# Kernel tuning notes

Hardware: AMD Instinct MI355X
Metric: run time of the kernel (lower is better)

## Reference

```python
import jax, jax.numpy as jnp
import numpy as np

C = 32                      # channels
DIMS = (8, 14, 18)          # basis_dim_per_atom for the 3 atom types
COUNTS = (8192, 8192, 4096) # number of atoms of each type


def setup_inputs() -> dict:
    key = jax.random.key(0)
    ks = iter(jax.random.split(key, 32))
    inp = {}
    N = sum(d * n for d, n in zip(DIMS, COUNTS))  # 253952 total basis rows
    inp["x"] = jax.random.normal(next(ks), (N, C), jnp.float32)
    c2 = C * C
    off = 0
    for t, (d, n) in enumerate(zip(DIMS, COUNTS)):
        rows = d * n
        # index array equivalent to the boolean atomic_number_mask for this type
        inp[f"idx{t}"] = jnp.arange(off, off + rows, dtype=jnp.int32)
        off += rows
        A = jax.random.normal(next(ks), (d, d), jnp.float32)
        inp[f"S{t}"] = 0.1 * (A + A.T)  # symmetric Coulomb/overlap matrix stand-in
        inp[f"W1_{t}"] = jax.random.normal(next(ks), (c2, c2), jnp.float32) * 0.03
        inp[f"b1_{t}"] = jnp.zeros((c2,), jnp.float32)
        inp[f"g{t}"] = jnp.ones((c2,), jnp.float32)
        inp[f"beta{t}"] = jnp.zeros((c2,), jnp.float32)
        inp[f"W2_{t}"] = jax.random.normal(next(ks), (c2, c2), jnp.float32) * 0.03
        inp[f"b2_{t}"] = jnp.zeros((c2,), jnp.float32)
    return inp


def _atom_block(y, S, W1, b1, g, beta, W2, b2):
    # y: [n_atoms, d, C]
    n = y.shape[0]
    # l2 = einsum('ij,aic,ajm->acm', S, y, y)  -> [n, C, C]
    Sy = jnp.einsum('ij,ajm->aim', S, y)
    l2 = jnp.einsum('aic,aim->acm', y, Sy)
    h = l2.reshape(n, C * C)
    # MLP: Linear -> SiLU -> LayerNorm -> Linear
    h = jax.nn.silu(h @ W1.T + b1)
    mu = jnp.mean(h, axis=-1, keepdims=True)
    var = jnp.var(h, axis=-1, keepdims=True)
    h = (h - mu) * jax.lax.rsqrt(var + 1e-5) * g + beta
    l2 = (h @ W2.T + b2).reshape(n, C, C)
    # x = x @ l2 per atom
    return jnp.einsum('aic,acm->aim', y, l2)


def reference(x, idx0, idx1, idx2,
              S0, W1_0, b1_0, g0, beta0, W2_0, b2_0,
              S1, W1_1, b1_1, g1, beta1, W2_1, b2_1,
              S2, W1_2, b1_2, g2, beta2, W2_2, b2_2):
    idxs = (idx0, idx1, idx2)
    params = ((S0, W1_0, b1_0, g0, beta0, W2_0, b2_0),
              (S1, W1_1, b1_1, g1, beta1, W2_1, b2_1),
              (S2, W1_2, b1_2, g2, beta2, W2_2, b2_2))
    for t in range(3):  # fixed small loop over atom types (structurally distinct)
        d = DIMS[t]
        y = x[idxs[t]].reshape(-1, d, C)          # gather + view per atom
        out = _atom_block(y, *params[t])          # per-type sub-module
        x = x.at[idxs[t]].set(out.reshape(-1, C)) # scatter back
    return x
```

## Files before the change

kernel.cpp:

```cpp
#include <hip/hip_runtime.h>
#include <math.h>

#define C2 1024

typedef float f32x4 __attribute__((ext_vector_type(4)));
typedef _Float16 f16x8 __attribute__((ext_vector_type(8)));
typedef unsigned short u16x8 __attribute__((ext_vector_type(8)));

__device__ __forceinline__ unsigned short f2h(float f) {
    _Float16 h = (_Float16)f;
    return __builtin_bit_cast(unsigned short, h);
}

__device__ __forceinline__ void gload16(const void* g, void* l) {
    __builtin_amdgcn_global_load_lds((const __attribute__((address_space(1))) void*)g,
                                     (__attribute__((address_space(3))) void*)l,
                                     16, 0, 0);
}

__device__ __forceinline__ int type_of(int pos, int s1, int s2) {
    return (pos >= s2) ? 2 : (pos >= s1) ? 1 : 0;
}
__device__ __forceinline__ int dim_of(int t) { return (t == 0) ? 8 : (t == 1) ? 14 : 18; }

__global__ __launch_bounds__(256) void k_conv(const float* __restrict__ s0, const float* __restrict__ s1,
                                              const float* __restrict__ s2, const float* __restrict__ s3,
                                              const float* __restrict__ s4, const float* __restrict__ s5,
                                              unsigned short* __restrict__ w) {
    int mat = blockIdx.x >> 10, bb = blockIdx.x & 1023;
    const float* src = (mat == 0) ? s0 : (mat == 1) ? s1 : (mat == 2) ? s2
                       : (mat == 3) ? s3 : (mat == 4) ? s4 : s5;
    int i = (bb * 256 + threadIdx.x) * 4;
    unsigned short* dst = w + (size_t)mat * 1048576;
    float4 v = *(const float4*)(src + i);
    ushort4 h;
    h.x = f2h(v.x); h.y = f2h(v.y); h.z = f2h(v.z); h.w = f2h(v.w);
    *(ushort4*)(dst + i) = h;
}

__global__ __launch_bounds__(256) void k_l2(const float* __restrict__ x,
                                            const int* __restrict__ i0, const int* __restrict__ i1,
                                            const int* __restrict__ i2,
                                            const float* __restrict__ S0, const float* __restrict__ S1,
                                            const float* __restrict__ S2,
                                            unsigned short* __restrict__ Ah,
                                            int s1, int s2) {
    __shared__ float sS[324];
    __shared__ float sy[4][18][32];
    __shared__ float sSy[4][18][32];
    const int tid = threadIdx.x, g = tid >> 6, lane = tid & 63;
    const int a0 = blockIdx.x * 4;
    const int t = type_of(a0, s1, s2);
    const int d = dim_of(t);
    const int* idx = (t == 0) ? i0 : (t == 1) ? i1 : i2;
    const float* S = (t == 0) ? S0 : (t == 1) ? S1 : S2;
    const int start = (t == 0) ? 0 : (t == 1) ? s1 : s2;
    const int dd = d * d;
    for (int i = tid; i < dd; i += 256) sS[i] = S[i];
    const int a = a0 + g, la = a - start;
    const int nf4 = d * 8;
    for (int k = lane; k < nf4; k += 64) {
        int bi = k >> 3, f4 = (k & 7) * 4;
        int r = idx[la * d + bi];
        *(float4*)&sy[g][bi][f4] = *(const float4*)(x + (size_t)r * 32 + f4);
    }
    __syncthreads();
    for (int k = lane; k < d * 32; k += 64) {
        int i = k >> 5, m = k & 31;
        float acc = 0.f;
        for (int j = 0; j < d; ++j) acc += sS[i * d + j] * sy[g][j][m];
        sSy[g][i][m] = acc;
    }
    __syncthreads();
    const int c = lane >> 1, mb = (lane & 1) * 16;
    float acc[16];
#pragma unroll
    for (int mm = 0; mm < 16; ++mm) acc[mm] = 0.f;
    for (int i = 0; i < d; ++i) {
        float yc = sy[g][i][c];
#pragma unroll
        for (int mm = 0; mm < 16; ++mm) acc[mm] += yc * sSy[g][i][mb + mm];
    }
    u16x8 h0, h1;
#pragma unroll
    for (int mm = 0; mm < 8; ++mm) h0[mm] = f2h(acc[mm]);
#pragma unroll
    for (int mm = 0; mm < 8; ++mm) h1[mm] = f2h(acc[8 + mm]);
    size_t off = (size_t)a * C2 + lane * 16;
    *(u16x8*)(Ah + off) = h0;
    *(u16x8*)(Ah + off + 8) = h1;
}

template <int DO_SILU>
__global__ __launch_bounds__(256) void k_gemm_mfma(const unsigned short* __restrict__ A,
                                                   const unsigned short* __restrict__ W0,
                                                   const unsigned short* __restrict__ W1,
                                                   const unsigned short* __restrict__ W2,
                                                   const float* __restrict__ bias0, const float* __restrict__ bias1,
                                                   const float* __restrict__ bias2,
                                                   float* __restrict__ Out, int tb1, int tb2) {
    __shared__ short lds[8192];
    short* As = lds;
    short* Ws = lds + 4096;

    const int tid = threadIdx.x;
    const int wid = tid >> 6, lane = tid & 63;
    const int bm = blockIdx.x, bn = blockIdx.y;
    const int wr = wid >> 1, wc = wid & 1;

    const unsigned short* W; const float* bias;
    if (bm >= tb2)      { W = W2; bias = bias2; }
    else if (bm >= tb1) { W = W1; bias = bias1; }
    else                { W = W0; bias = bias0; }

    size_t gA[2], gW[2];
    int ldsoff[2];
#pragma unroll
    for (int it = 0; it < 2; ++it) {
        int L = wid * 128 + it * 64 + lane;
        int row = L >> 2, slot = L & 3;
        int sw = slot ^ ((row >> 1) & 3);
        gA[it] = (size_t)(bm * 128 + row) * C2 + sw * 8;
        gW[it] = (size_t)(bn * 128 + row) * C2 + sw * 8;
        ldsoff[it] = wid * 1024 + it * 512;
    }

    const int col = lane & 15, g = lane >> 4;
    int aoffs[4], woffs[4];
#pragma unroll
    for (int i = 0; i < 4; ++i) {
        int ra = wr * 64 + i * 16 + col;
        aoffs[i] = ra * 32 + (g ^ ((ra >> 1) & 3)) * 8;
        int rw = wc * 64 + i * 16 + col;
        woffs[i] = rw * 32 + (g ^ ((rw >> 1) & 3)) * 8;
    }

    f32x4 acc[4][4] = {};

    for (int k0 = 0; k0 < C2; k0 += 32) {
#pragma unroll
        for (int it = 0; it < 2; ++it) {
            gload16(A + gA[it] + k0, As + ldsoff[it]);
            gload16(W + gW[it] + k0, Ws + ldsoff[it]);
        }
        __syncthreads();
        f16x8 ah[4], wh[4];
#pragma unroll
        for (int i = 0; i < 4; ++i) {
            ah[i] = *(const f16x8*)(As + aoffs[i]);
            wh[i] = *(const f16x8*)(Ws + woffs[i]);
        }
#pragma unroll
        for (int mi = 0; mi < 4; ++mi)
#pragma unroll
            for (int ni = 0; ni < 4; ++ni)
                acc[mi][ni] = __builtin_amdgcn_mfma_f32_16x16x32_f16(ah[mi], wh[ni], acc[mi][ni], 0, 0, 0);
        __syncthreads();
    }

    float bv[4];
#pragma unroll
    for (int ni = 0; ni < 4; ++ni) bv[ni] = bias[bn * 128 + wc * 64 + ni * 16 + col];
#pragma unroll
    for (int mi = 0; mi < 4; ++mi)
#pragma unroll
        for (int ni = 0; ni < 4; ++ni) {
            int n = bn * 128 + wc * 64 + ni * 16 + col;
#pragma unroll
            for (int r = 0; r < 4; ++r) {
                int m = bm * 128 + wr * 64 + mi * 16 + g * 4 + r;
                float v = acc[mi][ni][r] + bv[ni];
                if (DO_SILU) v = v / (1.f + __expf(-v));
                Out[(size_t)m * C2 + n] = v;
            }
        }
}

__global__ __launch_bounds__(256) void k_ln(const float* __restrict__ H,
                                            const float* __restrict__ g0, const float* __restrict__ g1,
                                            const float* __restrict__ g2,
                                            const float* __restrict__ b0, const float* __restrict__ b1,
                                            const float* __restrict__ b2,
                                            unsigned short* __restrict__ Bh,
                                            int s1, int s2) {
    const int tid = threadIdx.x, w = tid >> 6, lane = tid & 63;
    const int row = blockIdx.x * 4 + w;
    const int t = type_of(row, s1, s2);
    const float* gg = (t == 0) ? g0 : (t == 1) ? g1 : g2;
    const float* bb = (t == 0) ? b0 : (t == 1) ? b1 : b2;
    const float* rp = H + (size_t)row * C2;
    float4 v[4];
    float s = 0.f, s2v = 0.f;
#pragma unroll
    for (int k = 0; k < 4; ++k) {
        v[k] = *(const float4*)(rp + k * 256 + lane * 4);
        s += v[k].x + v[k].y + v[k].z + v[k].w;
        s2v += v[k].x * v[k].x + v[k].y * v[k].y + v[k].z * v[k].z + v[k].w * v[k].w;
    }
#pragma unroll
    for (int off = 1; off < 64; off <<= 1) {
        s += __shfl_xor(s, off);
        s2v += __shfl_xor(s2v, off);
    }
    float mean = s * (1.f / 1024.f);
    float var = s2v * (1.f / 1024.f) - mean * mean;
    float rstd = rsqrtf(var + 1e-5f);
#pragma unroll
    for (int k = 0; k < 4; ++k) {
        float4 gv = *(const float4*)(gg + k * 256 + lane * 4);
        float4 bv = *(const float4*)(bb + k * 256 + lane * 4);
        ushort4 h;
        h.x = f2h((v[k].x - mean) * rstd * gv.x + bv.x);
        h.y = f2h((v[k].y - mean) * rstd * gv.y + bv.y);
        h.z = f2h((v[k].z - mean) * rstd * gv.z + bv.z);
        h.w = f2h((v[k].w - mean) * rstd * gv.w + bv.w);
        size_t off2 = (size_t)row * C2 + k * 256 + lane * 4;
        *(ushort4*)(Bh + off2) = h;
    }
}

__global__ __launch_bounds__(256) void k_out(const float* __restrict__ x,
                                             const int* __restrict__ i0, const int* __restrict__ i1,
                                             const int* __restrict__ i2,
                                             const float* __restrict__ L,
                                             float* __restrict__ out, int s1, int s2) {
    __shared__ float sL[4][C2];
    __shared__ float sy[4][18][32];
    const int tid = threadIdx.x, g = tid >> 6, lane = tid & 63;
    const int a0 = blockIdx.x * 4;
    const int t = type_of(a0, s1, s2);
    const int d = dim_of(t);
    const int* idx = (t == 0) ? i0 : (t == 1) ? i1 : i2;
    const int start = (t == 0) ? 0 : (t == 1) ? s1 : s2;
    const int a = a0 + g, la = a - start;
    for (int k = lane; k < 256; k += 64)
        *(float4*)&sL[g][k * 4] = *(const float4*)(L + (size_t)a * C2 + k * 4);
    const int nf4 = d * 8;
    for (int k = lane; k < nf4; k += 64) {
        int bi = k >> 3, f4 = (k & 7) * 4;
        int r = idx[la * d + bi];
        *(float4*)&sy[g][bi][f4] = *(const float4*)(x + (size_t)r * 32 + f4);
    }
    __syncthreads();
    for (int k = lane; k < nf4; k += 64) {
        int bi = k >> 3, m4 = (k & 7) * 4;
        float ax = 0.f, ay = 0.f, az = 0.f, aw = 0.f;
#pragma unroll
        for (int c = 0; c < 32; ++c) {
            float yv = sy[g][bi][c];
            float4 lv = *(const float4*)&sL[g][c * 32 + m4];
            ax += yv * lv.x; ay += yv * lv.y; az += yv * lv.z; aw += yv * lv.w;
        }
        int r = idx[la * d + bi];
        float4 o = {ax, ay, az, aw};
        *(float4*)(out + (size_t)r * 32 + m4) = o;
    }
}

extern "C" void kernel_launch(void* const* d_in, const int* in_sizes, int n_in,
                              void* d_out, int out_size, void* d_ws, size_t ws_size,
                              hipStream_t stream) {
    const float* x = (const float*)d_in[0];
    static const int DIMS[3] = {8, 14, 18};
    static const int NATOMS[3] = {8192, 8192, 4096};
    const size_t MiB = 1ull << 20;
    const int BIG = 0x40000000;
    char* p = (char*)d_ws;

    const int* idxs[3]; const float* Ss[3]; const float* W1s[3]; const float* b1s[3];
    const float* gs[3]; const float* bes[3]; const float* W2s[3]; const float* b2s[3];
    for (int t = 0; t < 3; ++t) {
        idxs[t] = (const int*)d_in[1 + 8 * t];
        Ss[t] = (const float*)d_in[2 + 8 * t];
        W1s[t] = (const float*)d_in[3 + 8 * t];
        b1s[t] = (const float*)d_in[4 + 8 * t];
        gs[t] = (const float*)d_in[5 + 8 * t];
        bes[t] = (const float*)d_in[6 + 8 * t];
        W2s[t] = (const float*)d_in[7 + 8 * t];
        b2s[t] = (const float*)d_in[8 + 8 * t];
    }
    float* outp = (float*)d_out;

    if (ws_size >= 132 * MiB) {
        unsigned short* w = (unsigned short*)p;
        unsigned short* Ah = (unsigned short*)(p + 12 * MiB);
        float* H = (float*)(p + 52 * MiB);
        k_conv<<<6 * 1024, 256, 0, stream>>>(W1s[0], W2s[0], W1s[1], W2s[1], W1s[2], W2s[2], w);
        k_l2<<<5120, 256, 0, stream>>>(x, idxs[0], idxs[1], idxs[2], Ss[0], Ss[1], Ss[2],
                                       Ah, 8192, 16384);
        dim3 gg(160, 8);
        k_gemm_mfma<1><<<gg, 256, 0, stream>>>(Ah,
            w + 0 * 1048576, w + 2 * 1048576, w + 4 * 1048576,
            b1s[0], b1s[1], b1s[2], H, 64, 128);
        k_ln<<<5120, 256, 0, stream>>>(H, gs[0], gs[1], gs[2], bes[0], bes[1], bes[2],
                                       Ah, 8192, 16384);
        k_gemm_mfma<0><<<gg, 256, 0, stream>>>(Ah,
            w + 1 * 1048576, w + 3 * 1048576, w + 5 * 1048576,
            b2s[0], b2s[1], b2s[2], H, 64, 128);
        k_out<<<5120, 256, 0, stream>>>(x, idxs[0], idxs[1], idxs[2], H, outp, 8192, 16384);
    } else {
        unsigned short* wt = (unsigned short*)p;
        char* dyn = p + 4 * MiB;
        for (int t = 0; t < 3; ++t) {
            int n = NATOMS[t], d = DIMS[t];
            size_t fullneed = 4 * MiB + (size_t)n * 6144;
            int nch = (ws_size >= fullneed) ? 1 : 2;
            int cm = n / nch;
            unsigned short* Ah = (unsigned short*)dyn;
            float* Hbuf = (float*)(dyn + (size_t)cm * 2048);
            int ss1 = (t == 0) ? BIG : 0;
            int ss2 = (t == 2) ? 0 : BIG;
            k_conv<<<2 * 1024, 256, 0, stream>>>(W1s[t], W2s[t], W1s[t], W1s[t], W1s[t], W1s[t], wt);
            for (int ch = 0; ch < nch; ++ch) {
                const int* idxc = idxs[t] + (size_t)(ch * cm) * d;
                k_l2<<<cm / 4, 256, 0, stream>>>(x, idxc, idxc, idxc, Ss[t], Ss[t], Ss[t],
                                                 Ah, ss1, ss2);
                dim3 g1(cm / 128, 8);
                k_gemm_mfma<1><<<g1, 256, 0, stream>>>(Ah,
                    wt + 0, wt + 0, wt + 0,
                    b1s[t], b1s[t], b1s[t], Hbuf, BIG, BIG);
                k_ln<<<cm / 4, 256, 0, stream>>>(Hbuf, gs[t], gs[t], gs[t], bes[t], bes[t], bes[t],
                                                 Ah, ss1, ss2);
                k_gemm_mfma<0><<<g1, 256, 0, stream>>>(Ah,
                    wt + 1048576, wt + 1048576, wt + 1048576,
                    b2s[t], b2s[t], b2s[t], Hbuf, BIG, BIG);
                k_out<<<cm / 4, 256, 0, stream>>>(x, idxc, idxc, idxc, Hbuf, outp, ss1, ss2);
            }
        }
    }
    (void)in_sizes; (void)n_in; (void)out_size;
}
```

Before: 330.1 us.

## Store GEMM outputs as fp16 via LDS-staged coalesced writes

The two MLP GEMMs now write their intermediate activations in fp16 instead of fp32, and the epilogue stages each tile through padded LDS so global stores are 16-byte coalesced. LayerNorm and the output kernel read fp16 and convert back to fp32. This halves the intermediate activation traffic and removes scattered 4-byte stores, at the cost of extra epilogue syncs and reduced precision in the pre-LayerNorm and final l2 values.

Result: no change. 329.9 us (-0.1%).

```diff
diff --git a/kernel.cpp b/kernel.cpp
--- a/kernel.cpp
+++ b/kernel.cpp
@@ -10,6 +10,9 @@
 __device__ __forceinline__ unsigned short f2h(float f) {
     _Float16 h = (_Float16)f;
     return __builtin_bit_cast(unsigned short, h);
+}
+__device__ __forceinline__ float h2f(unsigned short u) {
+    return (float)__builtin_bit_cast(_Float16, u);
 }
 
 __device__ __forceinline__ void gload16(const void* g, void* l) {
@@ -98,8 +101,8 @@
                                                    const unsigned short* __restrict__ W2,
                                                    const float* __restrict__ bias0, const float* __restrict__ bias1,
                                                    const float* __restrict__ bias2,
-                                                   float* __restrict__ Out, int tb1, int tb2) {
-    __shared__ short lds[8192];
+                                                   unsigned short* __restrict__ Out, int tb1, int tb2) {
+    __shared__ short lds[8704];
     short* As = lds;
     short* Ws = lds + 4096;
 
@@ -161,22 +164,39 @@
     float bv[4];
 #pragma unroll
     for (int ni = 0; ni < 4; ++ni) bv[ni] = bias[bn * 128 + wc * 64 + ni * 16 + col];
-#pragma unroll
-    for (int mi = 0; mi < 4; ++mi)
-#pragma unroll
-        for (int ni = 0; ni < 4; ++ni) {
-            int n = bn * 128 + wc * 64 + ni * 16 + col;
-#pragma unroll
-            for (int r = 0; r < 4; ++r) {
-                int m = bm * 128 + wr * 64 + mi * 16 + g * 4 + r;
-                float v = acc[mi][ni][r] + bv[ni];
-                if (DO_SILU) v = v / (1.f + __expf(-v));
-                Out[(size_t)m * C2 + n] = v;
-            }
-        }
-}
-
-__global__ __launch_bounds__(256) void k_ln(const float* __restrict__ H,
+
+#pragma unroll
+    for (int hp = 0; hp < 2; ++hp) {
+        __syncthreads();
+#pragma unroll
+        for (int mh = 0; mh < 2; ++mh) {
+            int mi = hp * 2 + mh;
+#pragma unroll
+            for (int ni = 0; ni < 4; ++ni)
+#pragma unroll
+                for (int r = 0; r < 4; ++r) {
+                    float v = acc[mi][ni][r] + bv[ni];
+                    if (DO_SILU) v = v / (1.f + __expf(-v));
+                    int row = mh * 16 + g * 4 + r;
+                    int colc = wc * 64 + ni * 16 + col;
+                    lds[(wr * 32 + row) * 136 + colc] = (short)f2h(v);
+                }
+        }
+        __syncthreads();
+#pragma unroll
+        for (int i = 0; i < 4; ++i) {
+            int ci = tid + i * 256;
+            int wrp = ci >> 9, rem = ci & 511;
+            int row = rem >> 4, c8 = rem & 15;
+            u16x8 val = *(u16x8*)&lds[(wrp * 32 + row) * 136 + c8 * 8];
+            int grow = bm * 128 + wrp * 64 + hp * 32 + row;
+            int gcol = bn * 128 + c8 * 8;
+            *(u16x8*)&Out[(size_t)grow * C2 + gcol] = val;
+        }
+    }
+}
+
+__global__ __launch_bounds__(256) void k_ln(const unsigned short* __restrict__ H,
                                             const float* __restrict__ g0, const float* __restrict__ g1,
                                             const float* __restrict__ g2,
                                             const float* __restrict__ b0, const float* __restrict__ b1,
@@ -188,15 +208,17 @@
     const int t = type_of(row, s1, s2);
     const float* gg = (t == 0) ? g0 : (t == 1) ? g1 : g2;
     const float* bb = (t == 0) ? b0 : (t == 1) ? b1 : b2;
-    const float* rp = H + (size_t)row * C2;
-    float4 v[4];
+    const unsigned short* rp = H + (size_t)row * C2 + lane * 16;
+    u16x8 hv0 = *(const u16x8*)rp;
+    u16x8 hv1 = *(const u16x8*)(rp + 8);
+    float v[16];
+#pragma unroll
+    for (int k = 0; k < 8; ++k) v[k] = h2f(hv0[k]);
+#pragma unroll
+    for (int k = 0; k < 8; ++k) v[8 + k] = h2f(hv1[k]);
     float s = 0.f, s2v = 0.f;
 #pragma unroll
-    for (int k = 0; k < 4; ++k) {
-        v[k] = *(const float4*)(rp + k * 256 + lane * 4);
-        s += v[k].x + v[k].y + v[k].z + v[k].w;
-        s2v += v[k].x * v[k].x + v[k].y * v[k].y + v[k].z * v[k].z + v[k].w * v[k].w;
-    }
+    for (int k = 0; k < 16; ++k) { s += v[k]; s2v += v[k] * v[k]; }
 #pragma unroll
     for (int off = 1; off < 64; off <<= 1) {
         s += __shfl_xor(s, off);
@@ -205,24 +227,32 @@
     float mean = s * (1.f / 1024.f);
     float var = s2v * (1.f / 1024.f) - mean * mean;
     float rstd = rsqrtf(var + 1e-5f);
-#pragma unroll
-    for (int k = 0; k < 4; ++k) {
-        float4 gv = *(const float4*)(gg + k * 256 + lane * 4);
-        float4 bv = *(const float4*)(bb + k * 256 + lane * 4);
-        ushort4 h;
-        h.x = f2h((v[k].x - mean) * rstd * gv.x + bv.x);
-        h.y = f2h((v[k].y - mean) * rstd * gv.y + bv.y);
-        h.z = f2h((v[k].z - mean) * rstd * gv.z + bv.z);
-        h.w = f2h((v[k].w - mean) * rstd * gv.w + bv.w);
-        size_t off2 = (size_t)row * C2 + k * 256 + lane * 4;
-        *(ushort4*)(Bh + off2) = h;
-    }
+    u16x8 o0, o1;
+#pragma unroll
+    for (int q = 0; q < 4; ++q) {
+        float4 gv = *(const float4*)(gg + lane * 16 + q * 4);
+        float4 bv = *(const float4*)(bb + lane * 16 + q * 4);
+        float r0 = (v[q * 4 + 0] - mean) * rstd * gv.x + bv.x;
+        float r1 = (v[q * 4 + 1] - mean) * rstd * gv.y + bv.y;
+        float r2 = (v[q * 4 + 2] - mean) * rstd * gv.z + bv.z;
+        float r3 = (v[q * 4 + 3] - mean) * rstd * gv.w + bv.w;
+        if (q < 2) {
+            o0[q * 4 + 0] = f2h(r0); o0[q * 4 + 1] = f2h(r1);
+            o0[q * 4 + 2] = f2h(r2); o0[q * 4 + 3] = f2h(r3);
+        } else {
+            o1[(q - 2) * 4 + 0] = f2h(r0); o1[(q - 2) * 4 + 1] = f2h(r1);
+            o1[(q - 2) * 4 + 2] = f2h(r2); o1[(q - 2) * 4 + 3] = f2h(r3);
+        }
+    }
+    unsigned short* op = Bh + (size_t)row * C2 + lane * 16;
+    *(u16x8*)op = o0;
+    *(u16x8*)(op + 8) = o1;
 }
 
 __global__ __launch_bounds__(256) void k_out(const float* __restrict__ x,
                                              const int* __restrict__ i0, const int* __restrict__ i1,
                                              const int* __restrict__ i2,
-                                             const float* __restrict__ L,
+                                             const unsigned short* __restrict__ L,
                                              float* __restrict__ out, int s1, int s2) {
     __shared__ float sL[4][C2];
     __shared__ float sy[4][18][32];
@@ -233,8 +263,11 @@
     const int* idx = (t == 0) ? i0 : (t == 1) ? i1 : i2;
     const int start = (t == 0) ? 0 : (t == 1) ? s1 : s2;
     const int a = a0 + g, la = a - start;
-    for (int k = lane; k < 256; k += 64)
-        *(float4*)&sL[g][k * 4] = *(const float4*)(L + (size_t)a * C2 + k * 4);
+    for (int k = lane; k < 128; k += 64) {
+        u16x8 hv = *(const u16x8*)(L + (size_t)a * C2 + k * 8);
+#pragma unroll
+        for (int q = 0; q < 8; ++q) sL[g][k * 8 + q] = h2f(hv[q]);
+    }
     const int nf4 = d * 8;
     for (int k = lane; k < nf4; k += 64) {
         int bi = k >> 3, f4 = (k & 7) * 4;
@@ -281,10 +314,10 @@
     }
     float* outp = (float*)d_out;
 
-    if (ws_size >= 132 * MiB) {
+    if (ws_size >= 92 * MiB) {
         unsigned short* w = (unsigned short*)p;
         unsigned short* Ah = (unsigned short*)(p + 12 * MiB);
-        float* H = (float*)(p + 52 * MiB);
+        unsigned short* H = (unsigned short*)(p + 52 * MiB);
         k_conv<<<6 * 1024, 256, 0, stream>>>(W1s[0], W2s[0], W1s[1], W2s[1], W1s[2], W2s[2], w);
         k_l2<<<5120, 256, 0, stream>>>(x, idxs[0], idxs[1], idxs[2], Ss[0], Ss[1], Ss[2],
                                        Ah, 8192, 16384);
@@ -303,11 +336,11 @@
         char* dyn = p + 4 * MiB;
         for (int t = 0; t < 3; ++t) {
             int n = NATOMS[t], d = DIMS[t];
-            size_t fullneed = 4 * MiB + (size_t)n * 6144;
+            size_t fullneed = 4 * MiB + (size_t)n * 4096;
             int nch = (ws_size >= fullneed) ? 1 : 2;
             int cm = n / nch;
             unsigned short* Ah = (unsigned short*)dyn;
-            float* Hbuf = (float*)(dyn + (size_t)cm * 2048);
+            unsigned short* Hbuf = (unsigned short*)(dyn + (size_t)cm * 2048);
             int ss1 = (t == 0) ? BIG : 0;
             int ss2 = (t == 2) ? 0 : BIG;
             k_conv<<<2 * 1024, 256, 0, stream>>>(W1s[t], W2s[t], W1s[t], W1s[t], W1s[t], W1s[t], wt);
```
